# Performance work log

Measured on AMD Instinct MI355X. Metric: run time of the kernel, lower is better.

The kernel has to match this reference:

```python
import jax, jax.numpy as jnp
import numpy as np

B, T, C = 16, 4096, 128
CODEBOOK_SIZE = 1024


def setup_inputs() -> dict:
    key = jax.random.key(0)
    kx, ke = jax.random.split(key)
    x = jax.random.normal(kx, (B, T, C), dtype=jnp.float32)
    embed = jax.random.normal(ke, (CODEBOOK_SIZE, C), dtype=jnp.float32)
    return {"x": x, "embed": embed}


def reference(x, embed):
    # x: [B, T, C], embed: [K, C]
    b, t, c = x.shape
    flat = x.reshape(b * t, c)                      # [BT, C]
    # distance = -||x - e||^2, expanded so we never materialize [BT, K, C]
    x_sq = jnp.sum(flat * flat, axis=-1, keepdims=True)   # [BT, 1]
    e_sq = jnp.sum(embed * embed, axis=-1)                 # [K]
    dist = 2.0 * (flat @ embed.T) - x_sq - e_sq[None, :]   # [BT, K]
    embed_ind = jnp.argmax(dist, axis=-1).reshape(b, t)    # [B, T]
    quantized = embed[embed_ind]                           # [B, T, C] gather
    return quantized, embed_ind
```

## Files before the change

kernel.cpp:

```cpp
#include <hip/hip_runtime.h>
#include <float.h>


#define Cdim        128
#define KCODES      1024
#define CH          64
#define NCH         16
#define BROWS       128
#define THREADS     256
#define IMG_OFF     4096
#define CHUNK_BYTES 32768

typedef _Float16 f16;
typedef __attribute__((ext_vector_type(8))) _Float16 f16x8;
typedef __attribute__((ext_vector_type(4))) float    f32x4;

#define MFMA16(A, B, C) __builtin_amdgcn_mfma_f32_16x16x32_f16((A), (B), (C), 0, 0, 0)

__global__ __launch_bounds__(256) void esq_kernel(const float* __restrict__ embed,
                                                  float* __restrict__ esq, int K) {
    int gid  = blockIdx.x * blockDim.x + threadIdx.x;
    int code = gid >> 6;
    int lane = threadIdx.x & 63;
    if (code >= K) return;
    float2 v = ((const float2*)(embed + (size_t)code * Cdim))[lane];
    float  s = fmaf(v.x, v.x, v.y * v.y);
    #pragma unroll
    for (int m = 32; m >= 1; m >>= 1) s += __shfl_xor(s, m, 64);
    if (lane == 0) esq[code] = s;
}

__device__ __forceinline__ void cvt8s(float4 a, float4 b, float scale,
                                      f16x8& h, f16x8& lo) {
    float v[8] = {a.x, a.y, a.z, a.w, b.x, b.y, b.z, b.w};
    #pragma unroll
    for (int i = 0; i < 8; ++i) {
        float s = v[i] * scale;
        f16 hh = (f16)s;
        h[i]  = hh;
        lo[i] = (f16)(s - (float)hh);
    }
}

__global__ __launch_bounds__(256) void bconv_kernel(const float* __restrict__ embed,
                                                    char* __restrict__ ws) {
    int t    = blockIdx.x * 256 + threadIdx.x;
    int code = t >> 4;
    int seg  = t & 15;
    int ks   = seg >> 2;
    int kseg = seg & 3;
    int ch = code >> 6, ctg = (code >> 4) & 3, lr = code & 15;
    const float4* p = (const float4*)(embed + (size_t)code * Cdim + ks * 32 + kseg * 8);
    f16x8 h, lo;
    cvt8s(p[0], p[1], 1.0f, h, lo);
    size_t base = (size_t)IMG_OFF + (size_t)ch * CHUNK_BYTES
                + (ctg * 4 + ks) * 1024 + (kseg * 16 + lr) * 16;
    *(f16x8*)(ws + base)         = h;
    *(f16x8*)(ws + base + 16384) = lo;
}

__device__ __forceinline__ void gll16(const void* g, void* l) {
    __builtin_amdgcn_global_load_lds(
        (const __attribute__((address_space(1))) unsigned int*)g,
        (__attribute__((address_space(3))) unsigned int*)l, 16, 0, 0);
}

__global__ __launch_bounds__(THREADS, 2) void vq_kernel(
    const float* __restrict__ x, const float* __restrict__ embed,
    const char* __restrict__ ws, float* __restrict__ outq,
    float* __restrict__ outi) {

    __shared__ __align__(16) char  Bb[2][CHUNK_BYTES];
    __shared__ __align__(16) float esq_lds[KCODES];
    __shared__ float mrg_v[2][BROWS];
    __shared__ int   mrg_i[2][BROWS];
    __shared__ int   winners[BROWS];

    const int tid  = threadIdx.x;
    const int wid  = tid >> 6;
    const int l    = tid & 63;
    const int lr   = l & 15;
    const int lg   = l >> 4;
    const int wr   = wid & 1;
    const int nt   = wid >> 1;
    const int row0 = blockIdx.x * BROWS;

    {
        const char* src = ws + IMG_OFF + wid * 8192 + (size_t)l * 16;
        char*       dst = &Bb[0][wid * 8192];
        #pragma unroll
        for (int i = 0; i < 8; ++i) gll16(src + i * 1024, dst + i * 1024);
        gll16(ws + wid * 1024 + (size_t)l * 16, (char*)esq_lds + wid * 1024);
    }

    f16x8 bxh[4][4], bxl[4][4];
    #pragma unroll
    for (int rt = 0; rt < 4; ++rt) {
        const float* xr = x + (size_t)(row0 + wr * 64 + rt * 16 + lr) * Cdim + lg * 8;
        #pragma unroll
        for (int ks = 0; ks < 4; ++ks) {
            float4 v0 = *(const float4*)(xr + ks * 32);
            float4 v1 = *(const float4*)(xr + ks * 32 + 4);
            cvt8s(v0, v1, 2.0f, bxh[rt][ks], bxl[rt][ks]);
        }
    }

    float best[4];
    int   bidx[4];
    #pragma unroll
    for (int rt = 0; rt < 4; ++rt) { best[rt] = -FLT_MAX; bidx[rt] = 0; }

    #pragma unroll 1
    for (int ch = 0; ch < NCH; ++ch) {
        const int cur = ch & 1, nxt = cur ^ 1;

        __builtin_amdgcn_s_barrier();
        if (ch + 1 < NCH) {
            const char* src = ws + IMG_OFF + (size_t)(ch + 1) * CHUNK_BYTES
                            + wid * 8192 + (size_t)l * 16;
            char* dst = &Bb[nxt][wid * 8192];
            #pragma unroll
            for (int i = 0; i < 8; ++i) gll16(src + i * 1024, dst + i * 1024);
            asm volatile("s_waitcnt vmcnt(8)" ::: "memory");
        } else {
            asm volatile("s_waitcnt vmcnt(0)" ::: "memory");
        }
        __builtin_amdgcn_s_barrier();

        f32x4 acc[2][4];
        #pragma unroll
        for (int ct = 0; ct < 2; ++ct)
            #pragma unroll
            for (int rt = 0; rt < 4; ++rt)
                acc[ct][rt] = (f32x4){0.f, 0.f, 0.f, 0.f};

        const char* bb = &Bb[cur][(size_t)l * 16];

        #pragma unroll
        for (int ks = 0; ks < 4; ++ks) {
            f16x8 eh0 = *(const f16x8*)(bb + ((nt * 2 + 0) * 4 + ks) * 1024);
            f16x8 el0 = *(const f16x8*)(bb + ((nt * 2 + 0) * 4 + ks) * 1024 + 16384);
            f16x8 eh1 = *(const f16x8*)(bb + ((nt * 2 + 1) * 4 + ks) * 1024);
            f16x8 el1 = *(const f16x8*)(bb + ((nt * 2 + 1) * 4 + ks) * 1024 + 16384);

            __builtin_amdgcn_s_setprio(1);
            #pragma unroll
            for (int rt = 0; rt < 4; ++rt) acc[0][rt] = MFMA16(eh0, bxh[rt][ks], acc[0][rt]);
            #pragma unroll
            for (int rt = 0; rt < 4; ++rt) acc[1][rt] = MFMA16(eh1, bxh[rt][ks], acc[1][rt]);
            #pragma unroll
            for (int rt = 0; rt < 4; ++rt) acc[0][rt] = MFMA16(eh0, bxl[rt][ks], acc[0][rt]);
            #pragma unroll
            for (int rt = 0; rt < 4; ++rt) acc[1][rt] = MFMA16(eh1, bxl[rt][ks], acc[1][rt]);
            #pragma unroll
            for (int rt = 0; rt < 4; ++rt) acc[0][rt] = MFMA16(el0, bxh[rt][ks], acc[0][rt]);
            #pragma unroll
            for (int rt = 0; rt < 4; ++rt) acc[1][rt] = MFMA16(el1, bxh[rt][ks], acc[1][rt]);
            __builtin_amdgcn_s_setprio(0);
        }

        #pragma unroll
        for (int ct = 0; ct < 2; ++ct) {
            const int cb = ch * CH + (nt * 2 + ct) * 16 + lg * 4;
            float4 e4 = *(const float4*)&esq_lds[cb];
            #pragma unroll
            for (int rt = 0; rt < 4; ++rt) {
                #pragma unroll
                for (int j = 0; j < 4; ++j) {
                    float s = acc[ct][rt][j] - ((const float*)&e4)[j];
                    if (s > best[rt]) { best[rt] = s; bidx[rt] = cb + j; }
                }
            }
        }
    }

    #pragma unroll
    for (int rt = 0; rt < 4; ++rt) {
        float bs = best[rt]; int bi = bidx[rt];
        #pragma unroll
        for (int m = 16; m <= 32; m <<= 1) {
            float vs = __shfl_xor(bs, m, 64);
            int   vi = __shfl_xor(bi, m, 64);
            if (vs > bs || (vs == bs && vi < bi)) { bs = vs; bi = vi; }
        }
        if (lg == 0) {
            mrg_v[nt][wr * 64 + rt * 16 + lr] = bs;
            mrg_i[nt][wr * 64 + rt * 16 + lr] = bi;
        }
    }
    __syncthreads();
    if (tid < BROWS) {
        float v0 = mrg_v[0][tid]; int i0 = mrg_i[0][tid];
        float v1 = mrg_v[1][tid]; int i1 = mrg_i[1][tid];
        int bi = (v1 > v0 || (v1 == v0 && i1 < i0)) ? i1 : i0;
        winners[tid] = bi;
        outi[row0 + tid] = (float)bi;
    }
    __syncthreads();

    #pragma unroll
    for (int i = 0; i < 16; ++i) {
        int pos = i * THREADS + tid;
        int r = pos >> 5, c4 = pos & 31;
        int idx = winners[r];
        float4 v = ((const float4*)(embed + (size_t)idx * Cdim))[c4];
        ((float4*)(outq + (size_t)(row0 + r) * Cdim))[c4] = v;
    }
}

extern "C" void kernel_launch(void* const* d_in, const int* in_sizes, int n_in,
                              void* d_out, int out_size, void* d_ws, size_t ws_size,
                              hipStream_t stream) {
    const float* x     = (const float*)d_in[0];
    const float* embed = (const float*)d_in[1];
    const int M = in_sizes[0] / Cdim;
    const int K = in_sizes[1] / Cdim;
    float* outq = (float*)d_out;
    float* outi = outq + (size_t)M * Cdim;

    esq_kernel <<<K / 4, 256, 0, stream>>>(embed, (float*)d_ws, K);
    bconv_kernel<<<64, 256, 0, stream>>>(embed, (char*)d_ws);
    vq_kernel  <<<M / BROWS, THREADS, 0, stream>>>(x, embed, (const char*)d_ws,
                                                   outq, outi);
}
```

Measured before the change: 61.44 us.

## Triple-buffer smaller codebook chunks and give each wave its own row slice

Halves the codebook chunk to 32 codes and uses a 3-deep LDS ring with prefetch distance two, leaving one barrier per iteration instead of two. Each wave now owns 32 rows and scans all codes, so the cross-wave argmax merge through LDS goes away. e_sq is read straight from global memory rather than staged in LDS. In exchange there are twice as many chunk iterations, and every wave reads the whole chunk from LDS, so total LDS read traffic per block doubles.

```diff
diff --git a/kernel.cpp b/kernel.cpp
--- a/kernel.cpp
+++ b/kernel.cpp
@@ -4,12 +4,12 @@
 
 #define Cdim        128
 #define KCODES      1024
-#define CH          64
-#define NCH         16
+#define CH          32
+#define NCH         32
 #define BROWS       128
 #define THREADS     256
 #define IMG_OFF     4096
-#define CHUNK_BYTES 32768
+#define CHUNK_BYTES 16384
 
 typedef _Float16 f16;
 typedef __attribute__((ext_vector_type(8))) _Float16 f16x8;
@@ -49,14 +49,14 @@
     int seg  = t & 15;
     int ks   = seg >> 2;
     int kseg = seg & 3;
-    int ch = code >> 6, ctg = (code >> 4) & 3, lr = code & 15;
+    int ch = code >> 5, ct = (code >> 4) & 1, lr = code & 15;
     const float4* p = (const float4*)(embed + (size_t)code * Cdim + ks * 32 + kseg * 8);
     f16x8 h, lo;
     cvt8s(p[0], p[1], 1.0f, h, lo);
     size_t base = (size_t)IMG_OFF + (size_t)ch * CHUNK_BYTES
-                + (ctg * 4 + ks) * 1024 + (kseg * 16 + lr) * 16;
-    *(f16x8*)(ws + base)         = h;
-    *(f16x8*)(ws + base + 16384) = lo;
+                + (ct * 4 + ks) * 1024 + (kseg * 16 + lr) * 16;
+    *(f16x8*)(ws + base)        = h;
+    *(f16x8*)(ws + base + 8192) = lo;
 }
 
 __device__ __forceinline__ void gll16(const void* g, void* l) {
@@ -70,33 +70,28 @@
     const char* __restrict__ ws, float* __restrict__ outq,
     float* __restrict__ outi) {
 
-    __shared__ __align__(16) char  Bb[2][CHUNK_BYTES];
-    __shared__ __align__(16) float esq_lds[KCODES];
-    __shared__ float mrg_v[2][BROWS];
-    __shared__ int   mrg_i[2][BROWS];
-    __shared__ int   winners[BROWS];
+    __shared__ __align__(16) char Bb[3][CHUNK_BYTES];
 
     const int tid  = threadIdx.x;
     const int wid  = tid >> 6;
     const int l    = tid & 63;
     const int lr   = l & 15;
     const int lg   = l >> 4;
-    const int wr   = wid & 1;
-    const int nt   = wid >> 1;
     const int row0 = blockIdx.x * BROWS;
-
-    {
-        const char* src = ws + IMG_OFF + wid * 8192 + (size_t)l * 16;
-        char*       dst = &Bb[0][wid * 8192];
-        #pragma unroll
-        for (int i = 0; i < 8; ++i) gll16(src + i * 1024, dst + i * 1024);
-        gll16(ws + wid * 1024 + (size_t)l * 16, (char*)esq_lds + wid * 1024);
-    }
-
-    f16x8 bxh[4][4], bxl[4][4];
-    #pragma unroll
-    for (int rt = 0; rt < 4; ++rt) {
-        const float* xr = x + (size_t)(row0 + wr * 64 + rt * 16 + lr) * Cdim + lg * 8;
+    const int wrow = row0 + wid * 32;
+
+    #pragma unroll
+    for (int b = 0; b < 2; ++b) {
+        const char* src = ws + IMG_OFF + b * CHUNK_BYTES + wid * 4096 + (size_t)l * 16;
+        char*       dst = &Bb[b][wid * 4096];
+        #pragma unroll
+        for (int i = 0; i < 4; ++i) gll16(src + i * 1024, dst + i * 1024);
+    }
+
+    f16x8 bxh[2][4], bxl[2][4];
+    #pragma unroll
+    for (int rt = 0; rt < 2; ++rt) {
+        const float* xr = x + (size_t)(wrow + rt * 16 + lr) * Cdim + lg * 8;
         #pragma unroll
         for (int ks = 0; ks < 4; ++ks) {
             float4 v0 = *(const float4*)(xr + ks * 32);
@@ -105,77 +100,79 @@
         }
     }
 
-    float best[4];
-    int   bidx[4];
-    #pragma unroll
-    for (int rt = 0; rt < 4; ++rt) { best[rt] = -FLT_MAX; bidx[rt] = 0; }
+    const float* esqp = (const float*)ws;
+
+    float best[2] = {-FLT_MAX, -FLT_MAX};
+    int   bidx[2] = {0, 0};
+    int cur = 0, pf = 2;
 
     #pragma unroll 1
     for (int ch = 0; ch < NCH; ++ch) {
-        const int cur = ch & 1, nxt = cur ^ 1;
-
+        if (ch == NCH - 1) asm volatile("s_waitcnt vmcnt(0)" ::: "memory");
+        else               asm volatile("s_waitcnt vmcnt(4)" ::: "memory");
         __builtin_amdgcn_s_barrier();
-        if (ch + 1 < NCH) {
-            const char* src = ws + IMG_OFF + (size_t)(ch + 1) * CHUNK_BYTES
-                            + wid * 8192 + (size_t)l * 16;
-            char* dst = &Bb[nxt][wid * 8192];
+
+        if (ch + 2 < NCH) {
+            const char* src = ws + IMG_OFF + (size_t)(ch + 2) * CHUNK_BYTES
+                            + wid * 4096 + (size_t)l * 16;
+            char* dst = &Bb[0][0] + (size_t)pf * CHUNK_BYTES + wid * 4096;
             #pragma unroll
-            for (int i = 0; i < 8; ++i) gll16(src + i * 1024, dst + i * 1024);
-            asm volatile("s_waitcnt vmcnt(8)" ::: "memory");
-        } else {
-            asm volatile("s_waitcnt vmcnt(0)" ::: "memory");
-        }
-        __builtin_amdgcn_s_barrier();
-
-        f32x4 acc[2][4];
+            for (int i = 0; i < 4; ++i) gll16(src + i * 1024, dst + i * 1024);
+        }
+
+        f32x4 acc[2][2];
         #pragma unroll
         for (int ct = 0; ct < 2; ++ct)
             #pragma unroll
-            for (int rt = 0; rt < 4; ++rt)
+            for (int rt = 0; rt < 2; ++rt)
                 acc[ct][rt] = (f32x4){0.f, 0.f, 0.f, 0.f};
 
-        const char* bb = &Bb[cur][(size_t)l * 16];
+        const char* bb = &Bb[0][0] + (size_t)cur * CHUNK_BYTES + (size_t)l * 16;
 
         #pragma unroll
         for (int ks = 0; ks < 4; ++ks) {
-            f16x8 eh0 = *(const f16x8*)(bb + ((nt * 2 + 0) * 4 + ks) * 1024);
-            f16x8 el0 = *(const f16x8*)(bb + ((nt * 2 + 0) * 4 + ks) * 1024 + 16384);
-            f16x8 eh1 = *(const f16x8*)(bb + ((nt * 2 + 1) * 4 + ks) * 1024);
-            f16x8 el1 = *(const f16x8*)(bb + ((nt * 2 + 1) * 4 + ks) * 1024 + 16384);
+            f16x8 eh0 = *(const f16x8*)(bb + ks * 1024);
+            f16x8 el0 = *(const f16x8*)(bb + ks * 1024 + 8192);
+            f16x8 eh1 = *(const f16x8*)(bb + (4 + ks) * 1024);
+            f16x8 el1 = *(const f16x8*)(bb + (4 + ks) * 1024 + 8192);
 
             __builtin_amdgcn_s_setprio(1);
+            acc[0][0] = MFMA16(eh0, bxh[0][ks], acc[0][0]);
+            acc[0][1] = MFMA16(eh0, bxh[1][ks], acc[0][1]);
+            acc[1][0] = MFMA16(eh1, bxh[0][ks], acc[1][0]);
+            acc[1][1] = MFMA16(eh1, bxh[1][ks], acc[1][1]);
+            acc[0][0] = MFMA16(eh0, bxl[0][ks], acc[0][0]);
+            acc[0][1] = MFMA16(eh0, bxl[1][ks], acc[0][1]);
+            acc[1][0] = MFMA16(eh1, bxl[0][ks], acc[1][0]);
+            acc[1][1] = MFMA16(eh1, bxl[1][ks], acc[1][1]);
+            acc[0][0] = MFMA16(el0, bxh[0][ks], acc[0][0]);
+            acc[0][1] = MFMA16(el0, bxh[1][ks], acc[0][1]);
+            acc[1][0] = MFMA16(el1, bxh[0][ks], acc[1][0]);
+            acc[1][1] = MFMA16(el1, bxh[1][ks], acc[1][1]);
+            __builtin_amdgcn_s_setprio(0);
+        }
+
+        #pragma unroll
+        for (int ct = 0; ct < 2; ++ct) {
+            const int cb = ch * CH + ct * 16 + lg * 4;
+            float4 e4 = *(const float4*)(esqp + cb);
             #pragma unroll
-            for (int rt = 0; rt < 4; ++rt) acc[0][rt] = MFMA16(eh0, bxh[rt][ks], acc[0][rt]);
-            #pragma unroll
-            for (int rt = 0; rt < 4; ++rt) acc[1][rt] = MFMA16(eh1, bxh[rt][ks], acc[1][rt]);
-            #pragma unroll
-            for (int rt = 0; rt < 4; ++rt) acc[0][rt] = MFMA16(eh0, bxl[rt][ks], acc[0][rt]);
-            #pragma unroll
-            for (int rt = 0; rt < 4; ++rt) acc[1][rt] = MFMA16(eh1, bxl[rt][ks], acc[1][rt]);
-            #pragma unroll
-            for (int rt = 0; rt < 4; ++rt) acc[0][rt] = MFMA16(el0, bxh[rt][ks], acc[0][rt]);
-            #pragma unroll
-            for (int rt = 0; rt < 4; ++rt) acc[1][rt] = MFMA16(el1, bxh[rt][ks], acc[1][rt]);
-            __builtin_amdgcn_s_setprio(0);
-        }
-
-        #pragma unroll
-        for (int ct = 0; ct < 2; ++ct) {
-            const int cb = ch * CH + (nt * 2 + ct) * 16 + lg * 4;
-            float4 e4 = *(const float4*)&esq_lds[cb];
-            #pragma unroll
-            for (int rt = 0; rt < 4; ++rt) {
+            for (int rt = 0; rt < 2; ++rt)
                 #pragma unroll
                 for (int j = 0; j < 4; ++j) {
                     float s = acc[ct][rt][j] - ((const float*)&e4)[j];
                     if (s > best[rt]) { best[rt] = s; bidx[rt] = cb + j; }
                 }
-            }
-        }
-    }
-
-    #pragma unroll
-    for (int rt = 0; rt < 4; ++rt) {
+        }
+
+        cur = (cur == 2) ? 0 : cur + 1;
+        pf  = (pf  == 2) ? 0 : pf  + 1;
+    }
+
+    __syncthreads();
+    int* winners = (int*)&Bb[0][0];
+    #pragma unroll
+    for (int rt = 0; rt < 2; ++rt) {
         float bs = best[rt]; int bi = bidx[rt];
         #pragma unroll
         for (int m = 16; m <= 32; m <<= 1) {
@@ -184,17 +181,9 @@
             if (vs > bs || (vs == bs && vi < bi)) { bs = vs; bi = vi; }
         }
         if (lg == 0) {
-            mrg_v[nt][wr * 64 + rt * 16 + lr] = bs;
-            mrg_i[nt][wr * 64 + rt * 16 + lr] = bi;
-        }
-    }
-    __syncthreads();
-    if (tid < BROWS) {
-        float v0 = mrg_v[0][tid]; int i0 = mrg_i[0][tid];
-        float v1 = mrg_v[1][tid]; int i1 = mrg_i[1][tid];
-        int bi = (v1 > v0 || (v1 == v0 && i1 < i0)) ? i1 : i0;
-        winners[tid] = bi;
-        outi[row0 + tid] = (float)bi;
+            winners[wid * 32 + rt * 16 + lr] = bi;
+            outi[wrow + rt * 16 + lr] = (float)bi;
+        }
     }
     __syncthreads();
 
```

Measured after the change: 62.43 us. Within noise of the previous version (+1.6%).

## Use 512-thread blocks with smaller per-wave tiles and split accumulators

Applied to the files above, without the earlier changes.

Doubles the threads per block to 8 waves, each handling 32 rows by 16 codes per chunk. The codebook chunk shrinks to 32 codes and is re-laid out to match. The three f16 split-precision products now accumulate into separate registers and are summed at the end, shortening the MFMA dependency chains. Register pressure drops so more waves can be resident and hide latency, at the cost of twice as many chunk iterations and barriers per block.

```diff
diff --git a/kernel.cpp b/kernel.cpp
--- a/kernel.cpp
+++ b/kernel.cpp
@@ -4,12 +4,12 @@
 
 #define Cdim        128
 #define KCODES      1024
-#define CH          64
-#define NCH         16
+#define CH          32
+#define NCH         32
 #define BROWS       128
-#define THREADS     256
+#define THREADS     512
 #define IMG_OFF     4096
-#define CHUNK_BYTES 32768
+#define CHUNK_BYTES 16384
 
 typedef _Float16 f16;
 typedef __attribute__((ext_vector_type(8))) _Float16 f16x8;
@@ -49,14 +49,14 @@
     int seg  = t & 15;
     int ks   = seg >> 2;
     int kseg = seg & 3;
-    int ch = code >> 6, ctg = (code >> 4) & 3, lr = code & 15;
+    int ch = code >> 5, nt = (code >> 4) & 1, lr = code & 15;
     const float4* p = (const float4*)(embed + (size_t)code * Cdim + ks * 32 + kseg * 8);
     f16x8 h, lo;
     cvt8s(p[0], p[1], 1.0f, h, lo);
     size_t base = (size_t)IMG_OFF + (size_t)ch * CHUNK_BYTES
-                + (ctg * 4 + ks) * 1024 + (kseg * 16 + lr) * 16;
-    *(f16x8*)(ws + base)         = h;
-    *(f16x8*)(ws + base + 16384) = lo;
+                + nt * 8192 + ks * 1024 + (kseg * 16 + lr) * 16;
+    *(f16x8*)(ws + base)        = h;
+    *(f16x8*)(ws + base + 4096) = lo;
 }
 
 __device__ __forceinline__ void gll16(const void* g, void* l) {
@@ -65,15 +65,15 @@
         (__attribute__((address_space(3))) unsigned int*)l, 16, 0, 0);
 }
 
-__global__ __launch_bounds__(THREADS, 2) void vq_kernel(
+__global__ __launch_bounds__(THREADS, 4) void vq_kernel(
     const float* __restrict__ x, const float* __restrict__ embed,
     const char* __restrict__ ws, float* __restrict__ outq,
     float* __restrict__ outi) {
 
     __shared__ __align__(16) char  Bb[2][CHUNK_BYTES];
     __shared__ __align__(16) float esq_lds[KCODES];
-    __shared__ float mrg_v[2][BROWS];
-    __shared__ int   mrg_i[2][BROWS];
+    __shared__ float mrgv[2][BROWS];
+    __shared__ int   mrgi[2][BROWS];
     __shared__ int   winners[BROWS];
 
     const int tid  = threadIdx.x;
@@ -81,22 +81,22 @@
     const int l    = tid & 63;
     const int lr   = l & 15;
     const int lg   = l >> 4;
-    const int wr   = wid & 1;
-    const int nt   = wid >> 1;
+    const int wr   = wid >> 1;
+    const int nt   = wid & 1;
     const int row0 = blockIdx.x * BROWS;
 
     {
-        const char* src = ws + IMG_OFF + wid * 8192 + (size_t)l * 16;
-        char*       dst = &Bb[0][wid * 8192];
-        #pragma unroll
-        for (int i = 0; i < 8; ++i) gll16(src + i * 1024, dst + i * 1024);
-        gll16(ws + wid * 1024 + (size_t)l * 16, (char*)esq_lds + wid * 1024);
-    }
-
-    f16x8 bxh[4][4], bxl[4][4];
-    #pragma unroll
-    for (int rt = 0; rt < 4; ++rt) {
-        const float* xr = x + (size_t)(row0 + wr * 64 + rt * 16 + lr) * Cdim + lg * 8;
+        const char* src = ws + IMG_OFF + wid * 1024 + (size_t)l * 16;
+        gll16(src,        &Bb[0][wid * 1024]);
+        gll16(src + 8192, &Bb[0][wid * 1024 + 8192]);
+        if (wid < 4)
+            gll16(ws + wid * 1024 + (size_t)l * 16, (char*)esq_lds + wid * 1024);
+    }
+
+    f16x8 bxh[2][4], bxl[2][4];
+    #pragma unroll
+    for (int rt = 0; rt < 2; ++rt) {
+        const float* xr = x + (size_t)(row0 + wr * 32 + rt * 16 + lr) * Cdim + lg * 8;
         #pragma unroll
         for (int ks = 0; ks < 4; ++ks) {
             float4 v0 = *(const float4*)(xr + ks * 32);
@@ -105,10 +105,8 @@
         }
     }
 
-    float best[4];
-    int   bidx[4];
-    #pragma unroll
-    for (int rt = 0; rt < 4; ++rt) { best[rt] = -FLT_MAX; bidx[rt] = 0; }
+    float best[2] = {-FLT_MAX, -FLT_MAX};
+    int   bidx[2] = {0, 0};
 
     #pragma unroll 1
     for (int ch = 0; ch < NCH; ++ch) {
@@ -117,65 +115,51 @@
         __builtin_amdgcn_s_barrier();
         if (ch + 1 < NCH) {
             const char* src = ws + IMG_OFF + (size_t)(ch + 1) * CHUNK_BYTES
-                            + wid * 8192 + (size_t)l * 16;
-            char* dst = &Bb[nxt][wid * 8192];
-            #pragma unroll
-            for (int i = 0; i < 8; ++i) gll16(src + i * 1024, dst + i * 1024);
-            asm volatile("s_waitcnt vmcnt(8)" ::: "memory");
+                            + wid * 1024 + (size_t)l * 16;
+            gll16(src,        &Bb[nxt][wid * 1024]);
+            gll16(src + 8192, &Bb[nxt][wid * 1024 + 8192]);
+            asm volatile("s_waitcnt vmcnt(2)" ::: "memory");
         } else {
             asm volatile("s_waitcnt vmcnt(0)" ::: "memory");
         }
         __builtin_amdgcn_s_barrier();
 
-        f32x4 acc[2][4];
-        #pragma unroll
-        for (int ct = 0; ct < 2; ++ct)
+        f32x4 a1[2], a2[2], a3[2];
+        #pragma unroll
+        for (int rt = 0; rt < 2; ++rt) {
+            a1[rt] = (f32x4){0.f, 0.f, 0.f, 0.f};
+            a2[rt] = (f32x4){0.f, 0.f, 0.f, 0.f};
+            a3[rt] = (f32x4){0.f, 0.f, 0.f, 0.f};
+        }
+
+        const char* bb = &Bb[cur][nt * 8192 + (size_t)l * 16];
+        #pragma unroll
+        for (int ks = 0; ks < 4; ++ks) {
+            f16x8 eh = *(const f16x8*)(bb + ks * 1024);
+            f16x8 el = *(const f16x8*)(bb + 4096 + ks * 1024);
+            __builtin_amdgcn_s_setprio(1);
+            a1[0] = MFMA16(eh, bxh[0][ks], a1[0]);
+            a1[1] = MFMA16(eh, bxh[1][ks], a1[1]);
+            a2[0] = MFMA16(eh, bxl[0][ks], a2[0]);
+            a2[1] = MFMA16(eh, bxl[1][ks], a2[1]);
+            a3[0] = MFMA16(el, bxh[0][ks], a3[0]);
+            a3[1] = MFMA16(el, bxh[1][ks], a3[1]);
+            __builtin_amdgcn_s_setprio(0);
+        }
+
+        const int cb = ch * CH + nt * 16 + lg * 4;
+        float4 e4 = *(const float4*)&esq_lds[cb];
+        #pragma unroll
+        for (int rt = 0; rt < 2; ++rt)
             #pragma unroll
-            for (int rt = 0; rt < 4; ++rt)
-                acc[ct][rt] = (f32x4){0.f, 0.f, 0.f, 0.f};
-
-        const char* bb = &Bb[cur][(size_t)l * 16];
-
-        #pragma unroll
-        for (int ks = 0; ks < 4; ++ks) {
-            f16x8 eh0 = *(const f16x8*)(bb + ((nt * 2 + 0) * 4 + ks) * 1024);
-            f16x8 el0 = *(const f16x8*)(bb + ((nt * 2 + 0) * 4 + ks) * 1024 + 16384);
-            f16x8 eh1 = *(const f16x8*)(bb + ((nt * 2 + 1) * 4 + ks) * 1024);
-            f16x8 el1 = *(const f16x8*)(bb + ((nt * 2 + 1) * 4 + ks) * 1024 + 16384);
-
-            __builtin_amdgcn_s_setprio(1);
-            #pragma unroll
-            for (int rt = 0; rt < 4; ++rt) acc[0][rt] = MFMA16(eh0, bxh[rt][ks], acc[0][rt]);
-            #pragma unroll
-            for (int rt = 0; rt < 4; ++rt) acc[1][rt] = MFMA16(eh1, bxh[rt][ks], acc[1][rt]);
-            #pragma unroll
-            for (int rt = 0; rt < 4; ++rt) acc[0][rt] = MFMA16(eh0, bxl[rt][ks], acc[0][rt]);
-            #pragma unroll
-            for (int rt = 0; rt < 4; ++rt) acc[1][rt] = MFMA16(eh1, bxl[rt][ks], acc[1][rt]);
-            #pragma unroll
-            for (int rt = 0; rt < 4; ++rt) acc[0][rt] = MFMA16(el0, bxh[rt][ks], acc[0][rt]);
-            #pragma unroll
-            for (int rt = 0; rt < 4; ++rt) acc[1][rt] = MFMA16(el1, bxh[rt][ks], acc[1][rt]);
-            __builtin_amdgcn_s_setprio(0);
-        }
-
-        #pragma unroll
-        for (int ct = 0; ct < 2; ++ct) {
-            const int cb = ch * CH + (nt * 2 + ct) * 16 + lg * 4;
-            float4 e4 = *(const float4*)&esq_lds[cb];
-            #pragma unroll
-            for (int rt = 0; rt < 4; ++rt) {
-                #pragma unroll
-                for (int j = 0; j < 4; ++j) {
-                    float s = acc[ct][rt][j] - ((const float*)&e4)[j];
-                    if (s > best[rt]) { best[rt] = s; bidx[rt] = cb + j; }
-                }
+            for (int j = 0; j < 4; ++j) {
+                float s = ((a1[rt][j] + a2[rt][j]) + a3[rt][j]) - ((const float*)&e4)[j];
+                if (s > best[rt]) { best[rt] = s; bidx[rt] = cb + j; }
             }
-        }
-    }
-
-    #pragma unroll
-    for (int rt = 0; rt < 4; ++rt) {
+    }
+
+    #pragma unroll
+    for (int rt = 0; rt < 2; ++rt) {
         float bs = best[rt]; int bi = bidx[rt];
         #pragma unroll
         for (int m = 16; m <= 32; m <<= 1) {
@@ -184,14 +168,14 @@
             if (vs > bs || (vs == bs && vi < bi)) { bs = vs; bi = vi; }
         }
         if (lg == 0) {
-            mrg_v[nt][wr * 64 + rt * 16 + lr] = bs;
-            mrg_i[nt][wr * 64 + rt * 16 + lr] = bi;
+            mrgv[nt][wr * 32 + rt * 16 + lr] = bs;
+            mrgi[nt][wr * 32 + rt * 16 + lr] = bi;
         }
     }
     __syncthreads();
     if (tid < BROWS) {
-        float v0 = mrg_v[0][tid]; int i0 = mrg_i[0][tid];
-        float v1 = mrg_v[1][tid]; int i1 = mrg_i[1][tid];
+        float v0 = mrgv[0][tid]; int i0 = mrgi[0][tid];
+        float v1 = mrgv[1][tid]; int i1 = mrgi[1][tid];
         int bi = (v1 > v0 || (v1 == v0 && i1 < i0)) ? i1 : i0;
         winners[tid] = bi;
         outi[row0 + tid] = (float)bi;
@@ -199,7 +183,7 @@
     __syncthreads();
 
     #pragma unroll
-    for (int i = 0; i < 16; ++i) {
+    for (int i = 0; i < 8; ++i) {
         int pos = i * THREADS + tid;
         int r = pos >> 5, c4 = pos & 31;
         int idx = winners[r];
```

New measurement: 65.44 us. 1.07x slower.
